# Performance work log

Hardware: AMD Instinct MI355X
Metric: run time of the kernel (lower is better)

The kernel has to match this reference:

```python
import jax, jax.numpy as jnp
import numpy as np

B, T_OUT, L, D, H = 1, 8, 512, 512, 8  # batch, frames, tokens/frame, d_model, heads


def setup_inputs() -> dict:
    key = jax.random.key(0)
    ks = jax.random.split(key, 7)
    return {
        "hidden_states": jax.random.normal(ks[0], (B * T_OUT, L, D), jnp.float32),
        "p_out": jax.random.normal(ks[1], (B, T_OUT, 4, 4), jnp.float32),
        "p_out_inv": jax.random.normal(ks[2], (B, T_OUT, 4, 4), jnp.float32),
        "Wq": jax.random.normal(ks[3], (D, D), jnp.float32) * 0.02,
        "Wk": jax.random.normal(ks[4], (D, D), jnp.float32) * 0.02,
        "Wv": jax.random.normal(ks[5], (D, D), jnp.float32) * 0.02,
        "Wo": jax.random.normal(ks[6], (D, D), jnp.float32) * 0.02,
        "bo": jnp.zeros((D,), jnp.float32),
        "num_heads": H,
    }


def cape_embed(f, P):
    # f: (b, S, d), P: (b, S, 4, 4); rearrange '(d k)'->'d k' with k=4, matmul by P, flatten back
    b, S, d = f.shape
    f4 = f.reshape(b, S, d // 4, 4)
    return jnp.einsum('bsdk,bskg->bsdg', f4, P).reshape(b, S, d)


def reference(hidden_states, p_out, p_out_inv, Wq, Wk, Wv, Wo, bo, num_heads):
    b, t_out = p_out.shape[0], p_out.shape[1]
    bt, l, d = hidden_states.shape
    S = t_out * l
    residual = hidden_states

    # '(b t_out) l d -> b (t_out l) d'
    x = hidden_states.reshape(b, S, d)

    q = x @ Wq
    k = x @ Wk
    v = x @ Wv

    # repeat per-frame CAPE matrices over tokens within each frame; self-attn so p_in = p_out
    Pq = jnp.repeat(p_out_inv, l, axis=1)  # (b, S, 4, 4)
    Pk = jnp.repeat(p_out, l, axis=1)      # (b, S, 4, 4)
    q = cape_embed(q, Pq)
    k = cape_embed(k, Pk)

    hd = d // num_heads
    scale = hd ** -0.5
    qh = q.reshape(b, S, num_heads, hd).transpose(0, 2, 1, 3)  # (b, h, S, hd)
    kh = k.reshape(b, S, num_heads, hd).transpose(0, 2, 1, 3)
    vh = v.reshape(b, S, num_heads, hd).transpose(0, 2, 1, 3)

    scores = jnp.einsum('bhqd,bhkd->bhqk', qh, kh) * scale  # full (b,h,S,S) matrix
    probs = jax.nn.softmax(scores, axis=-1)
    o = jnp.einsum('bhqk,bhkd->bhqd', probs, vh)

    o = o.transpose(0, 2, 1, 3).reshape(b, S, d)
    o = o @ Wo + bo  # to_out[0]; to_out[1] dropout is identity in eval

    # 'b (t_out l) d -> (b t_out) l d'
    o = o.reshape(bt, l, d)
    return o + residual  # residual_connection; rescale_output_factor = 1.0
```

## Files before the change

### kernel.cpp

```cpp
#include <hip/hip_runtime.h>
#include <hip/hip_bf16.h>
#include <stdint.h>

typedef __bf16 bf16_t;
typedef __bf16 bf16x2 __attribute__((ext_vector_type(2)));
typedef __bf16 bf16x4 __attribute__((ext_vector_type(4)));
typedef __bf16 bf16x8 __attribute__((ext_vector_type(8)));
typedef float f32x4 __attribute__((ext_vector_type(4)));

#define MFMA(a, b, c) __builtin_amdgcn_mfma_f32_16x16x32_bf16(a, b, c, 0, 0, 0)

#if __has_builtin(__builtin_amdgcn_exp2f)
#define FEXP2 __builtin_amdgcn_exp2f
#else
#define FEXP2 exp2f
#endif

__device__ __forceinline__ void g2lds16(const void* g, void* l) {
  __builtin_amdgcn_global_load_lds(
      reinterpret_cast<const __attribute__((address_space(1))) unsigned int*>(
          reinterpret_cast<uintptr_t>(g)),
      reinterpret_cast<__attribute__((address_space(3))) unsigned int*>(
          reinterpret_cast<uintptr_t>(l)),
      16, 0, 0);
}

__global__ __launch_bounds__(256) void k_prep(const float* __restrict__ x,
                                              const float* __restrict__ Wq,
                                              const float* __restrict__ Wk,
                                              const float* __restrict__ Wv,
                                              const float* __restrict__ Wo,
                                              const float* __restrict__ Pout,
                                              const float* __restrict__ Pinv,
                                              bf16_t* __restrict__ Xbf,
                                              bf16_t* __restrict__ WqT,
                                              bf16_t* __restrict__ WkT,
                                              bf16_t* __restrict__ WvT,
                                              bf16_t* __restrict__ WoT) {
  const int bid = blockIdx.x;
  if (bid < 2048) {
    int i = (bid * 256 + threadIdx.x) * 4;
    float4 v = *reinterpret_cast<const float4*>(x + i);
    bf16x4 o;
    o[0] = (bf16_t)v.x; o[1] = (bf16_t)v.y; o[2] = (bf16_t)v.z; o[3] = (bf16_t)v.w;
    *reinterpret_cast<bf16x4*>(Xbf + i) = o;
  } else if (bid < 3072) {
    int idx = (bid - 2048) * 256 + threadIdx.x;
    int t = idx >> 15;
    int n = (idx >> 6) & 511;
    int k0 = (idx & 63) << 3;
    int dq4 = (n >> 2) << 2;
    int g = n & 3;
    float pq[4], pk[4];
#pragma unroll
    for (int h = 0; h < 4; ++h) {
      pq[h] = Pinv[t * 16 + h * 4 + g];
      pk[h] = Pout[t * 16 + h * 4 + g];
    }
    bf16x8 oq, ok;
#pragma unroll
    for (int j = 0; j < 8; ++j) {
      const float4 wq = *reinterpret_cast<const float4*>(Wq + (size_t)(k0 + j) * 512 + dq4);
      const float4 wk = *reinterpret_cast<const float4*>(Wk + (size_t)(k0 + j) * 512 + dq4);
      oq[j] = (bf16_t)((wq.x * pq[0] + wq.y * pq[1] + wq.z * pq[2] + wq.w * pq[3]) * 0.1803368801f);
      ok[j] = (bf16_t)(wk.x * pk[0] + wk.y * pk[1] + wk.z * pk[2] + wk.w * pk[3]);
    }
    size_t o = ((size_t)t * 512 + n) * 512 + k0;
    *reinterpret_cast<bf16x8*>(WqT + o) = oq;
    *reinterpret_cast<bf16x8*>(WkT + o) = ok;
  } else {
    int idx = (bid - 3072) * 256 + threadIdx.x;
    int mat = idx >> 15;
    int n = (idx >> 6) & 511;
    int k0 = (idx & 63) << 3;
    const float* W = mat ? Wo : Wv;
    bf16_t* T = mat ? WoT : WvT;
    bf16x8 o;
#pragma unroll
    for (int j = 0; j < 8; ++j) o[j] = (bf16_t)W[(size_t)(k0 + j) * 512 + n];
    *reinterpret_cast<bf16x8*>(T + (size_t)n * 512 + k0) = o;
  }
}

__global__ __launch_bounds__(256) void k_gemm_qkv(const bf16_t* __restrict__ Xbf,
                                                  const bf16_t* __restrict__ WqT,
                                                  const bf16_t* __restrict__ WkT,
                                                  const bf16_t* __restrict__ WvT,
                                                  bf16_t* __restrict__ Qh,
                                                  bf16_t* __restrict__ Kh,
                                                  bf16_t* __restrict__ Vt) {
  __shared__ bf16_t lA[128 * 64];
  __shared__ bf16_t lB[64 * 64];
  const int m0 = blockIdx.x * 128, n0 = blockIdx.y * 64;
  const int mat = blockIdx.z;
  const int frame = m0 >> 9;
  const bf16_t* WT = (mat == 0) ? (WqT + (size_t)frame * 512 * 512)
                   : (mat == 1) ? (WkT + (size_t)frame * 512 * 512)
                                : WvT;
  const int tid = threadIdx.x, lane = tid & 63, wid = tid >> 6;
  const int wr = wid >> 1, wc = wid & 1;
  const int l15 = lane & 15, lg = lane >> 4;
  const int srow = lane >> 3;
  const int scol = ((lane & 7) ^ (lane >> 3)) << 3;

  f32x4 acc[4][2] = {};

  for (int kt = 0; kt < 512; kt += 64) {
#pragma unroll
    for (int i = 0; i < 4; ++i) {
      int chunk = wid * 4 + i;
      int row = chunk * 8 + srow;
      g2lds16(Xbf + (size_t)(m0 + row) * 512 + kt + scol, lA + chunk * 512);
    }
#pragma unroll
    for (int i = 0; i < 2; ++i) {
      int chunk = wid * 2 + i;
      int row = chunk * 8 + srow;
      g2lds16(WT + (size_t)(n0 + row) * 512 + kt + scol, lB + chunk * 512);
    }
    __syncthreads();
#pragma unroll
    for (int kk = 0; kk < 2; ++kk) {
      bf16x8 af[4], bw[2];
      int c16 = ((4 * kk + lg) ^ (l15 & 7)) << 3;
#pragma unroll
      for (int i = 0; i < 4; ++i)
        af[i] = *reinterpret_cast<const bf16x8*>(lA + (wr * 64 + i * 16 + l15) * 64 + c16);
#pragma unroll
      for (int j = 0; j < 2; ++j)
        bw[j] = *reinterpret_cast<const bf16x8*>(lB + (wc * 32 + j * 16 + l15) * 64 + c16);
#pragma unroll
      for (int i = 0; i < 4; ++i)
#pragma unroll
        for (int j = 0; j < 2; ++j)
          acc[i][j] = MFMA(af[i], bw[j], acc[i][j]);
    }
    __syncthreads();
  }

#pragma unroll
  for (int i = 0; i < 4; ++i)
#pragma unroll
    for (int j = 0; j < 2; ++j)
#pragma unroll
      for (int r = 0; r < 4; ++r) {
        int s = m0 + wr * 64 + i * 16 + lg * 4 + r;
        int n = n0 + wc * 32 + j * 16 + l15;
        bf16_t v = (bf16_t)acc[i][j][r];
        if (mat == 2) {
          Vt[(size_t)n * 4096 + s] = v;
        } else if (mat == 0) {
          Qh[((size_t)(n >> 6) * 4096 + s) * 64 + (n & 63)] = v;
        } else {
          Kh[((size_t)(n >> 6) * 4096 + s) * 64 + (n & 63)] = v;
        }
      }
}

__global__ __launch_bounds__(256, 4) void k_attn(const bf16_t* __restrict__ Qh,
                                                 const bf16_t* __restrict__ Kh,
                                                 const bf16_t* __restrict__ Vt,
                                                 char* __restrict__ wsb,
                                                 float* __restrict__ Mp,
                                                 float* __restrict__ Lp) {
  __shared__ bf16_t lK[64 * 64];
  __shared__ bf16_t lV[64 * 64];
  __shared__ bf16_t lP[4 * 16 * 64];
  const int h = blockIdx.y;
  const int ks = blockIdx.z;
  const int q0 = blockIdx.x * 128;
  const int tid = threadIdx.x, lane = tid & 63, wid = tid >> 6;
  const int l15 = lane & 15, lg = lane >> 4;
  const int srow = lane >> 3;
  const int scol = ((lane & 7) ^ (lane >> 3)) << 3;

  bf16_t* Op = (bf16_t*)(ks < 3 ? wsb + ((size_t)ks << 22) : wsb + (29u << 20));

  bf16x8 qf[2][2];
#pragma unroll
  for (int g = 0; g < 2; ++g) {
    const bf16_t* Qp = Qh + ((size_t)h * 4096 + q0 + wid * 32 + g * 16 + l15) * 64;
#pragma unroll
    for (int kk = 0; kk < 2; ++kk)
      qf[g][kk] = *reinterpret_cast<const bf16x8*>(Qp + kk * 32 + lg * 8);
  }

  bf16x8 onesf;
#pragma unroll
  for (int j = 0; j < 8; ++j) onesf[j] = (bf16_t)1.0f;

  const bf16_t* Kb = Kh + ((size_t)h * 4096 + ks * 1024) * 64;
  const bf16_t* Vb = Vt + (size_t)h * 64 * 4096 + ks * 1024;

  f32x4 oT[2][4] = {};
  f32x4 lac[2] = {};
  float m[2] = {-3e38f, -3e38f};
  bf16_t* Pw = lP + wid * 1024;

  for (int t = 0; t < 16; ++t) {
#pragma unroll
    for (int i = 0; i < 2; ++i) {
      int chunk = wid * 2 + i;
      int row = chunk * 8 + srow;
      g2lds16(Kb + (size_t)(t * 64 + row) * 64 + scol, lK + chunk * 512);
      g2lds16(Vb + (size_t)row * 4096 + t * 64 + scol, lV + chunk * 512);
    }
    __syncthreads();

    f32x4 st[2][4] = {};
    __builtin_amdgcn_s_setprio(1);
#pragma unroll
    for (int kk = 0; kk < 2; ++kk)
#pragma unroll
      for (int mb = 0; mb < 4; ++mb) {
        bf16x8 kf = *reinterpret_cast<const bf16x8*>(
            lK + (mb * 16 + l15) * 64 + (((kk * 4 + lg) ^ (l15 & 7)) << 3));
        st[0][mb] = MFMA(kf, qf[0][kk], st[0][mb]);
        st[1][mb] = MFMA(kf, qf[1][kk], st[1][mb]);
      }
    __builtin_amdgcn_s_setprio(0);

#pragma unroll
    for (int g = 0; g < 2; ++g) {
      float t0 = fmaxf(fmaxf(st[g][0][0], st[g][0][1]), fmaxf(st[g][0][2], st[g][0][3]));
      float t1 = fmaxf(fmaxf(st[g][1][0], st[g][1][1]), fmaxf(st[g][1][2], st[g][1][3]));
      float t2 = fmaxf(fmaxf(st[g][2][0], st[g][2][1]), fmaxf(st[g][2][2], st[g][2][3]));
      float t3 = fmaxf(fmaxf(st[g][3][0], st[g][3][1]), fmaxf(st[g][3][2], st[g][3][3]));
      float tmax = fmaxf(fmaxf(t0, t1), fmaxf(t2, t3));
      tmax = fmaxf(tmax, __shfl_xor(tmax, 16, 64));
      tmax = fmaxf(tmax, __shfl_xor(tmax, 32, 64));
      if (!__all(tmax <= m[g] + 8.f)) {
        float mnew = fmaxf(m[g], tmax);
        float corr = FEXP2(m[g] - mnew);
        m[g] = mnew;
        lac[g] *= corr;
#pragma unroll
        for (int hb = 0; hb < 4; ++hb) oT[g][hb] *= corr;
      }
#pragma unroll
      for (int mb = 0; mb < 4; ++mb)
#pragma unroll
        for (int r = 0; r < 4; ++r)
          st[g][mb][r] = FEXP2(st[g][mb][r] - m[g]);
    }

    bf16x8 pb[2][2];
#pragma unroll
    for (int g = 0; g < 2; ++g) {
#pragma unroll
      for (int mb = 0; mb < 4; ++mb) {
        int key0 = mb * 16 + lg * 4;
        int c16 = (key0 >> 3) ^ (l15 & 7);
        bf16_t* p = Pw + l15 * 64 + c16 * 8 + (key0 & 7);
        bf16x2 p01, p23;
        p01[0] = (bf16_t)st[g][mb][0]; p01[1] = (bf16_t)st[g][mb][1];
        p23[0] = (bf16_t)st[g][mb][2]; p23[1] = (bf16_t)st[g][mb][3];
        *reinterpret_cast<bf16x2*>(p) = p01;
        *reinterpret_cast<bf16x2*>(p + 2) = p23;
      }
#pragma unroll
      for (int kk = 0; kk < 2; ++kk)
        pb[g][kk] = *reinterpret_cast<const bf16x8*>(
            Pw + l15 * 64 + (((kk * 4 + lg) ^ (l15 & 7)) << 3));
    }

    __builtin_amdgcn_s_setprio(1);
#pragma unroll
    for (int kk = 0; kk < 2; ++kk) {
      lac[0] = MFMA(onesf, pb[0][kk], lac[0]);
      lac[1] = MFMA(onesf, pb[1][kk], lac[1]);
#pragma unroll
      for (int hb = 0; hb < 4; ++hb) {
        bf16x8 vf = *reinterpret_cast<const bf16x8*>(
            lV + (hb * 16 + l15) * 64 + (((kk * 4 + lg) ^ (l15 & 7)) << 3));
        oT[0][hb] = MFMA(vf, pb[0][kk], oT[0][hb]);
        oT[1][hb] = MFMA(vf, pb[1][kk], oT[1][hb]);
      }
    }
    __builtin_amdgcn_s_setprio(0);
    __syncthreads();
  }

#pragma unroll
  for (int g = 0; g < 2; ++g) {
    int q = q0 + wid * 32 + g * 16 + l15;
    size_t rbase = ((size_t)ks * 8 + h) * 4096 + q;
    size_t obase = ((size_t)h * 4096 + q) * 64;
    if (lg == 0) { Mp[rbase] = m[g]; Lp[rbase] = lac[g][0]; }
#pragma unroll
    for (int hb = 0; hb < 4; ++hb) {
      bf16x4 ov;
#pragma unroll
      for (int r = 0; r < 4; ++r) ov[r] = (bf16_t)oT[g][hb][r];
      *reinterpret_cast<bf16x4*>(Op + obase + hb * 16 + lg * 4) = ov;
    }
  }
}

__global__ __launch_bounds__(256) void k_merge(char* __restrict__ wsb,
                                               const float* __restrict__ Mp,
                                               const float* __restrict__ Lp,
                                               bf16_t* __restrict__ Obf) {
  int idx = blockIdx.x * 256 + threadIdx.x;
  int d4 = (idx & 15) << 2;
  int row = idx >> 4;
  float ms[4];
  float mstar = -3e38f;
#pragma unroll
  for (int s = 0; s < 4; ++s) {
    ms[s] = Mp[s * 32768 + row];
    mstar = fmaxf(mstar, ms[s]);
  }
  float l = 0.f;
  f32x4 o = {};
#pragma unroll
  for (int s = 0; s < 4; ++s) {
    const bf16_t* Ops = (const bf16_t*)(s < 3 ? wsb + ((size_t)s << 22) : wsb + (29u << 20));
    float w = FEXP2(ms[s] - mstar);
    l += w * Lp[s * 32768 + row];
    bf16x4 v = *reinterpret_cast<const bf16x4*>(Ops + (size_t)row * 64 + d4);
    o[0] += w * (float)v[0]; o[1] += w * (float)v[1];
    o[2] += w * (float)v[2]; o[3] += w * (float)v[3];
  }
  float rinv = 1.f / l;
  int h = row >> 12, q = row & 4095;
  bf16x4 ov;
#pragma unroll
  for (int r = 0; r < 4; ++r) ov[r] = (bf16_t)(o[r] * rinv);
  *reinterpret_cast<bf16x4*>(Obf + (size_t)q * 512 + h * 64 + d4) = ov;
}

__global__ __launch_bounds__(256) void k_gemm_out(const bf16_t* __restrict__ Obf,
                                                  const bf16_t* __restrict__ WoT,
                                                  const float* __restrict__ bo,
                                                  const float* __restrict__ resid,
                                                  float* __restrict__ out) {
  __shared__ bf16_t lA[64 * 64];
  __shared__ bf16_t lB[64 * 64];
  const int m0 = blockIdx.x * 64, n0 = blockIdx.y * 64;
  const int tid = threadIdx.x, lane = tid & 63, wid = tid >> 6;
  const int wr = wid >> 1, wc = wid & 1;
  const int l15 = lane & 15, lg = lane >> 4;
  const int srow = lane >> 3;
  const int scol = ((lane & 7) ^ (lane >> 3)) << 3;

  f32x4 acc[2][2] = {};

  for (int kt = 0; kt < 512; kt += 64) {
#pragma unroll
    for (int i = 0; i < 2; ++i) {
      int chunk = wid * 2 + i;
      int row = chunk * 8 + srow;
      g2lds16(Obf + (size_t)(m0 + row) * 512 + kt + scol, lA + chunk * 512);
      g2lds16(WoT + (size_t)(n0 + row) * 512 + kt + scol, lB + chunk * 512);
    }
    __syncthreads();
#pragma unroll
    for (int kk = 0; kk < 2; ++kk) {
      bf16x8 af[2], bw[2];
      int c16 = ((4 * kk + lg) ^ (l15 & 7)) << 3;
#pragma unroll
      for (int i = 0; i < 2; ++i) {
        af[i] = *reinterpret_cast<const bf16x8*>(lA + (wr * 32 + i * 16 + l15) * 64 + c16);
        bw[i] = *reinterpret_cast<const bf16x8*>(lB + (wc * 32 + i * 16 + l15) * 64 + c16);
      }
#pragma unroll
      for (int i = 0; i < 2; ++i)
#pragma unroll
        for (int j = 0; j < 2; ++j)
          acc[i][j] = MFMA(af[i], bw[j], acc[i][j]);
    }
    __syncthreads();
  }

#pragma unroll
  for (int i = 0; i < 2; ++i)
#pragma unroll
    for (int j = 0; j < 2; ++j)
#pragma unroll
      for (int r = 0; r < 4; ++r) {
        int s = m0 + wr * 32 + i * 16 + lg * 4 + r;
        int n = n0 + wc * 32 + j * 16 + l15;
        size_t o = (size_t)s * 512 + n;
        out[o] = acc[i][j][r] + bo[n] + resid[o];
      }
}

extern "C" void kernel_launch(void* const* d_in, const int* in_sizes, int n_in,
                              void* d_out, int out_size, void* d_ws, size_t ws_size,
                              hipStream_t stream) {
  const float* hs   = (const float*)d_in[0];
  const float* pout = (const float*)d_in[1];
  const float* pinv = (const float*)d_in[2];
  const float* Wq   = (const float*)d_in[3];
  const float* Wk   = (const float*)d_in[4];
  const float* Wv   = (const float*)d_in[5];
  const float* Wo   = (const float*)d_in[6];
  const float* bo   = (const float*)d_in[7];
  float* out = (float*)d_out;

  char* ws = (char*)d_ws;
  bf16_t* Xbf = (bf16_t*)(ws);
  bf16_t* WqT = (bf16_t*)(ws + (4u << 20));
  bf16_t* WkT = (bf16_t*)(ws + (8u << 20));
  bf16_t* WvT = (bf16_t*)(ws + (12u << 20));
  bf16_t* WoT = (bf16_t*)(ws + (12u << 20) + (512u << 10));
  bf16_t* Qh  = (bf16_t*)(ws + (13u << 20));
  bf16_t* Kh  = (bf16_t*)(ws + (17u << 20));
  bf16_t* Vt  = (bf16_t*)(ws + (21u << 20));
  bf16_t* Obf = (bf16_t*)(ws + (25u << 20));
  float*  Mp  = (float*)(ws + (33u << 20));
  float*  Lp  = (float*)(ws + (33u << 20) + (512u << 10));

  hipLaunchKernelGGL(k_prep, dim3(3328), dim3(256), 0, stream,
                     hs, Wq, Wk, Wv, Wo, pout, pinv, Xbf, WqT, WkT, WvT, WoT);
  hipLaunchKernelGGL(k_gemm_qkv, dim3(32, 8, 3), dim3(256), 0, stream,
                     Xbf, WqT, WkT, WvT, Qh, Kh, Vt);
  hipLaunchKernelGGL(k_attn, dim3(32, 8, 4), dim3(256), 0, stream, Qh, Kh, Vt, ws, Mp, Lp);
  hipLaunchKernelGGL(k_merge, dim3(2048), dim3(256), 0, stream, ws, Mp, Lp, Obf);
  hipLaunchKernelGGL(k_gemm_out, dim3(64, 8), dim3(256), 0, stream, Obf, WoT, bo, hs, out);
}
```

Baseline: 107.9 us.

## Double-buffer K/V tiles in LDS and build P fragments via permlane swaps

The attention kernel now keeps two LDS buffers for K and V and issues the loads for the next key tile before computing on the current one, so global-to-LDS traffic can overlap the MFMA work. The P matrix no longer round-trips through LDS. It is packed with v_cvt_pk_bf16_f32 and rearranged into the MFMA B-operand layout with permlane32/permlane16 swaps, which removes LDS stores and loads plus a scratch buffer. A risk is that the loop still has only one __syncthreads at the end of each iteration, so the async load into the other buffer may race with the wait and visibility semantics. The permlane lane mapping also has to match the earlier LDS layout exactly.

```diff
diff --git a/kernel.cpp b/kernel.cpp
--- a/kernel.cpp
+++ b/kernel.cpp
@@ -23,6 +23,34 @@
       reinterpret_cast<__attribute__((address_space(3))) unsigned int*>(
           reinterpret_cast<uintptr_t>(l)),
       16, 0, 0);
+}
+
+__device__ __forceinline__ unsigned cvtpk(float lo, float hi) {
+  unsigned r;
+  asm("v_cvt_pk_bf16_f32 %0, %1, %2" : "=v"(r) : "v"(lo), "v"(hi));
+  return r;
+}
+
+__device__ __forceinline__ void lane_swap32(unsigned& a, unsigned& b) {
+#if __has_builtin(__builtin_amdgcn_permlane32_swap)
+  typedef int i32x2 __attribute__((ext_vector_type(2)));
+  i32x2 r = __builtin_amdgcn_permlane32_swap((int)a, (int)b, false, false);
+  a = (unsigned)r[0];
+  b = (unsigned)r[1];
+#else
+  asm("v_permlane32_swap_b32 %0, %1" : "+v"(a), "+v"(b));
+#endif
+}
+
+__device__ __forceinline__ void lane_swap16(unsigned& a, unsigned& b) {
+#if __has_builtin(__builtin_amdgcn_permlane16_swap)
+  typedef int i32x2 __attribute__((ext_vector_type(2)));
+  i32x2 r = __builtin_amdgcn_permlane16_swap((int)a, (int)b, false, false);
+  a = (unsigned)r[0];
+  b = (unsigned)r[1];
+#else
+  asm("v_permlane16_swap_b32 %0, %1" : "+v"(a), "+v"(b));
+#endif
 }
 
 __global__ __launch_bounds__(256) void k_prep(const float* __restrict__ x,
@@ -163,9 +191,8 @@
                                                  char* __restrict__ wsb,
                                                  float* __restrict__ Mp,
                                                  float* __restrict__ Lp) {
-  __shared__ bf16_t lK[64 * 64];
-  __shared__ bf16_t lV[64 * 64];
-  __shared__ bf16_t lP[4 * 16 * 64];
+  __shared__ bf16_t lK[2][64 * 64];
+  __shared__ bf16_t lV[2][64 * 64];
   const int h = blockIdx.y;
   const int ks = blockIdx.z;
   const int q0 = blockIdx.x * 128;
@@ -195,17 +222,23 @@
   f32x4 oT[2][4] = {};
   f32x4 lac[2] = {};
   float m[2] = {-3e38f, -3e38f};
-  bf16_t* Pw = lP + wid * 1024;
-
-  for (int t = 0; t < 16; ++t) {
+
+  auto stage = [&](int buf, int kt) {
 #pragma unroll
     for (int i = 0; i < 2; ++i) {
       int chunk = wid * 2 + i;
       int row = chunk * 8 + srow;
-      g2lds16(Kb + (size_t)(t * 64 + row) * 64 + scol, lK + chunk * 512);
-      g2lds16(Vb + (size_t)row * 4096 + t * 64 + scol, lV + chunk * 512);
-    }
-    __syncthreads();
+      g2lds16(Kb + (size_t)(kt + row) * 64 + scol, &lK[buf][chunk * 512]);
+      g2lds16(Vb + (size_t)row * 4096 + kt + scol, &lV[buf][chunk * 512]);
+    }
+  };
+
+  stage(0, 0);
+  __syncthreads();
+
+  for (int t = 0; t < 16; ++t) {
+    const int cur = t & 1;
+    if (t < 15) stage(cur ^ 1, (t + 1) * 64);
 
     f32x4 st[2][4] = {};
     __builtin_amdgcn_s_setprio(1);
@@ -214,7 +247,7 @@
 #pragma unroll
       for (int mb = 0; mb < 4; ++mb) {
         bf16x8 kf = *reinterpret_cast<const bf16x8*>(
-            lK + (mb * 16 + l15) * 64 + (((kk * 4 + lg) ^ (l15 & 7)) << 3));
+            &lK[cur][(mb * 16 + l15) * 64 + (((kk * 4 + lg) ^ (l15 & 7)) << 3)]);
         st[0][mb] = MFMA(kf, qf[0][kk], st[0][mb]);
         st[1][mb] = MFMA(kf, qf[1][kk], st[1][mb]);
       }
@@ -246,23 +279,21 @@
 
     bf16x8 pb[2][2];
 #pragma unroll
-    for (int g = 0; g < 2; ++g) {
-#pragma unroll
-      for (int mb = 0; mb < 4; ++mb) {
-        int key0 = mb * 16 + lg * 4;
-        int c16 = (key0 >> 3) ^ (l15 & 7);
-        bf16_t* p = Pw + l15 * 64 + c16 * 8 + (key0 & 7);
-        bf16x2 p01, p23;
-        p01[0] = (bf16_t)st[g][mb][0]; p01[1] = (bf16_t)st[g][mb][1];
-        p23[0] = (bf16_t)st[g][mb][2]; p23[1] = (bf16_t)st[g][mb][3];
-        *reinterpret_cast<bf16x2*>(p) = p01;
-        *reinterpret_cast<bf16x2*>(p + 2) = p23;
-      }
-#pragma unroll
-      for (int kk = 0; kk < 2; ++kk)
-        pb[g][kk] = *reinterpret_cast<const bf16x8*>(
-            Pw + l15 * 64 + (((kk * 4 + lg) ^ (l15 & 7)) << 3));
-    }
+    for (int g = 0; g < 2; ++g)
+#pragma unroll
+      for (int kk = 0; kk < 2; ++kk) {
+        unsigned A  = cvtpk(st[g][2 * kk][0],     st[g][2 * kk][1]);
+        unsigned Ap = cvtpk(st[g][2 * kk][2],     st[g][2 * kk][3]);
+        unsigned B  = cvtpk(st[g][2 * kk + 1][0], st[g][2 * kk + 1][1]);
+        unsigned Bp = cvtpk(st[g][2 * kk + 1][2], st[g][2 * kk + 1][3]);
+        lane_swap32(A, B);
+        lane_swap16(A, B);
+        lane_swap32(Ap, Bp);
+        lane_swap16(Ap, Bp);
+        union { unsigned u[4]; bf16x8 v; } pu;
+        pu.u[0] = A; pu.u[1] = Ap; pu.u[2] = B; pu.u[3] = Bp;
+        pb[g][kk] = pu.v;
+      }
 
     __builtin_amdgcn_s_setprio(1);
 #pragma unroll
@@ -272,7 +303,7 @@
 #pragma unroll
       for (int hb = 0; hb < 4; ++hb) {
         bf16x8 vf = *reinterpret_cast<const bf16x8*>(
-            lV + (hb * 16 + l15) * 64 + (((kk * 4 + lg) ^ (l15 & 7)) << 3));
+            &lV[cur][(hb * 16 + l15) * 64 + (((kk * 4 + lg) ^ (l15 & 7)) << 3)]);
         oT[0][hb] = MFMA(vf, pb[0][kk], oT[0][hb]);
         oT[1][hb] = MFMA(vf, pb[1][kk], oT[1][hb]);
       }
```

New measurement: 107.4 us. No clear change (-0.4%).
